# Kernel optimization log

Hardware: AMD Instinct MI355X
Metric: run time of the kernel (lower is better)

Reference implementation:

```python
import jax, jax.numpy as jnp
from jax import lax
import numpy as np

D_MODEL = 1024
D_STATE = 16
D_CONV = 4
EXPAND = 2
D_INNER = EXPAND * D_MODEL          # 2048
DT_RANK = (D_MODEL + 15) // 16      # 64
B_SZ, SEQ = 2, 2048


def setup_inputs() -> dict:
    key = jax.random.key(0)
    ks = jax.random.split(key, 10)
    s = 0.02
    x = jax.random.normal(ks[0], (B_SZ, SEQ, D_MODEL), jnp.float32)
    ln_w = jnp.ones((D_MODEL,), jnp.float32)
    ln_b = jnp.zeros((D_MODEL,), jnp.float32)
    in_proj_w = jax.random.normal(ks[1], (2 * D_INNER, D_MODEL), jnp.float32) * s
    conv_w = jax.random.normal(ks[2], (D_INNER, 1, D_CONV), jnp.float32) * s
    conv_b = jnp.zeros((D_INNER,), jnp.float32)
    x_proj_w = jax.random.normal(ks[3], (DT_RANK + 2 * D_STATE, D_INNER), jnp.float32) * s
    dt_proj_w = jax.random.normal(ks[4], (D_INNER, DT_RANK), jnp.float32) * s
    dt_proj_b = jax.random.normal(ks[5], (D_INNER,), jnp.float32) * s
    # standard Mamba S4D-real init: A = -[1..d_state] per channel
    A_log = jnp.log(jnp.tile(jnp.arange(1, D_STATE + 1, dtype=jnp.float32), (D_INNER, 1)))
    D_param = jnp.ones((D_INNER,), jnp.float32)
    out_proj_w = jax.random.normal(ks[6], (D_MODEL, D_INNER), jnp.float32) * s
    return dict(x=x, ln_w=ln_w, ln_b=ln_b, in_proj_w=in_proj_w, conv_w=conv_w,
                conv_b=conv_b, x_proj_w=x_proj_w, dt_proj_w=dt_proj_w,
                dt_proj_b=dt_proj_b, A_log=A_log, D_param=D_param,
                out_proj_w=out_proj_w)


def _mamba_layer(x, ln_w, ln_b, in_proj_w, conv_w, conv_b, x_proj_w,
                 dt_proj_w, dt_proj_b, A_log, D_param, out_proj_w):
    # LayerNorm (eps=1e-5)
    mu = x.mean(-1, keepdims=True)
    var = ((x - mu) ** 2).mean(-1, keepdims=True)
    xn = (x - mu) * lax.rsqrt(var + 1e-5) * ln_w + ln_b

    # input projection -> gate + conv branch
    xz = jnp.einsum('bld,ed->ble', xn, in_proj_w)  # [B,L,2*D_INNER]
    x_in, z = jnp.split(xz, 2, axis=-1)

    # causal depthwise conv1d + SiLU
    xc = lax.conv_general_dilated(x_in.transpose(0, 2, 1), conv_w, (1,),
                                  [(D_CONV - 1, 0)],
                                  dimension_numbers=('NCH', 'OIH', 'NCH'),
                                  feature_group_count=D_INNER)
    xc = jax.nn.silu(xc + conv_b[None, :, None]).transpose(0, 2, 1)  # [B,L,D_INNER]

    # SSM parameters
    dbl = jnp.einsum('bld,ed->ble', xc, x_proj_w)  # [B,L,DT_RANK+2N]
    dt, Bm, Cm = jnp.split(dbl, [DT_RANK, DT_RANK + D_STATE], axis=-1)
    delta = jax.nn.softplus(jnp.einsum('blr,dr->bld', dt, dt_proj_w) + dt_proj_b)
    A = -jnp.exp(A_log)  # [D_INNER, D_STATE]

    # selective scan over time
    def step(h, inp):
        d_t, B_t, C_t, u_t = inp  # [B,D_INNER],[B,N],[B,N],[B,D_INNER]
        dA = jnp.exp(d_t[..., None] * A)                         # [B,D_INNER,N]
        h = dA * h + (d_t * u_t)[..., None] * B_t[:, None, :]    # [B,D_INNER,N]
        y = jnp.einsum('bdn,bn->bd', h, C_t)
        return h, y

    h0 = jnp.zeros((x.shape[0], D_INNER, D_STATE), x.dtype)
    _, ys = lax.scan(step, h0, (delta.transpose(1, 0, 2), Bm.transpose(1, 0, 2),
                                Cm.transpose(1, 0, 2), xc.transpose(1, 0, 2)))
    y = ys.transpose(1, 0, 2) + xc * D_param   # [B,L,D_INNER]

    y = y * jax.nn.silu(z)
    out = jnp.einsum('ble,de->bld', y, out_proj_w)
    # dropout p=0 (eval) -> identity; residual
    return x + out


def reference(x, ln_w, ln_b, in_proj_w, conv_w, conv_b, x_proj_w,
              dt_proj_w, dt_proj_b, A_log, D_param, out_proj_w):
    return _mamba_layer(x, ln_w, ln_b, in_proj_w, conv_w, conv_b, x_proj_w,
                        dt_proj_w, dt_proj_b, A_log, D_param, out_proj_w)
```

## Files before the change

kernel.cpp:

```cpp
#include <hip/hip_runtime.h>
#include <hip/hip_bf16.h>
#include <math.h>

#define D_MODEL 1024
#define D_INNER 2048
#define DT_RANK 64
#define D_STATE 16
#define BSZ 2
#define SEQ 2048
#define NROW (BSZ * SEQ)
#define NC 128
#define CL (SEQ / NC)
#define NCH (BSZ * D_INNER)
#define KSPLIT 16
#define KCH (D_INNER / KSPLIT)
#define DSPLIT 4

typedef short bf16x8 __attribute__((ext_vector_type(8)));
typedef float f32x4 __attribute__((ext_vector_type(4)));

__device__ inline ushort f2bf(float f) {
    uint32_t u = __float_as_uint(f);
    return (ushort)((u + 0x7FFFu + ((u >> 16) & 1u)) >> 16);
}
__device__ inline float bf2f(ushort u) {
    return __uint_as_float(((uint32_t)u) << 16);
}

__device__ inline void gld_lds16(const void* g, void* l) {
    __builtin_amdgcn_global_load_lds(
        (__attribute__((address_space(1))) void*)g,
        (__attribute__((address_space(3))) void*)l, 16, 0, 0);
}

#define CVT_N1 (2 * D_INNER * D_MODEL / 4)
#define CVT_N2 (D_MODEL * D_INNER / 4)
#define CVT_N3 (D_INNER * DT_RANK / 4)
__global__ __launch_bounds__(256) void cvt_all(const float* __restrict__ a,
                                               const float* __restrict__ b,
                                               const float* __restrict__ c,
                                               ushort* __restrict__ oa,
                                               ushort* __restrict__ ob,
                                               ushort* __restrict__ oc) {
    int i = blockIdx.x * 256 + threadIdx.x;
    const float* src; ushort* dst; int j;
    if (i < CVT_N1)               { src = a; dst = oa; j = i; }
    else if (i < CVT_N1 + CVT_N2) { src = b; dst = ob; j = i - CVT_N1; }
    else                          { src = c; dst = oc; j = i - CVT_N1 - CVT_N2; }
    float4 v = ((const float4*)src)[j];
    ushort4 o;
    o.x = f2bf(v.x); o.y = f2bf(v.y); o.z = f2bf(v.z); o.w = f2bf(v.w);
    ((ushort4*)dst)[j] = o;
}

__global__ __launch_bounds__(256) void ln_kernel(const float* __restrict__ x,
                                                 const float* __restrict__ w,
                                                 const float* __restrict__ b,
                                                 ushort* __restrict__ xn) {
    int row = blockIdx.x;
    int tid = threadIdx.x;
    const float4* xr = (const float4*)(x + (size_t)row * D_MODEL);
    float4 v = xr[tid];
    float s  = v.x + v.y + v.z + v.w;
    float ss = v.x * v.x + v.y * v.y + v.z * v.z + v.w * v.w;
#pragma unroll
    for (int o = 32; o > 0; o >>= 1) {
        s  += __shfl_down(s, o);
        ss += __shfl_down(ss, o);
    }
    __shared__ float red[8];
    int wid = tid >> 6, lane = tid & 63;
    if (lane == 0) { red[wid] = s; red[4 + wid] = ss; }
    __syncthreads();
    s  = red[0] + red[1] + red[2] + red[3];
    ss = red[4] + red[5] + red[6] + red[7];
    float mu  = s * (1.0f / D_MODEL);
    float var = ss * (1.0f / D_MODEL) - mu * mu;
    float inv = rsqrtf(var + 1e-5f);
    float4 wv = ((const float4*)w)[tid];
    float4 bv = ((const float4*)b)[tid];
    ushort4 o4;
    o4.x = f2bf((v.x - mu) * inv * wv.x + bv.x);
    o4.y = f2bf((v.y - mu) * inv * wv.y + bv.y);
    o4.z = f2bf((v.z - mu) * inv * wv.z + bv.z);
    o4.w = f2bf((v.w - mu) * inv * wv.w + bv.w);
    ((ushort4*)(xn + (size_t)row * D_MODEL))[tid] = o4;
}

template <int MODE>
__global__ __launch_bounds__(256) void gemm_mfma(
    const ushort* __restrict__ A, int lda,
    const ushort* __restrict__ B, int ldb,
    float* __restrict__ C, ushort* __restrict__ Z0, ushort* __restrict__ Z1,
    int ldc, int splitN, const float* __restrict__ extra, int K, size_t zstride) {
    __shared__ ushort lds[2][2][128 * 32];
    int tid = threadIdx.x;
    int w = tid >> 6, lane = tid & 63;

    int nwg = gridDim.x * gridDim.y;
    int bid = blockIdx.y * gridDim.x + blockIdx.x;
    int cpx = nwg >> 3;
    int swz = (bid & 7) * cpx + (bid >> 3);
    int bx = swz % gridDim.x, by = swz / gridDim.x;
    int bm = by * 128, bn = bx * 128;
    int wr = w >> 1, wc = w & 1;

    int kofs = (MODE == 3) ? blockIdx.z * K : 0;
    int srow = tid >> 2, sseg = (tid & 3) << 3;
    const ushort* Abase = A + (size_t)(bm + srow) * lda + sseg + kofs;
    const ushort* Bbase = B + (size_t)(bn + srow) * ldb + sseg + kofs;
    int l0 = w * 512;

    int frow = lane & 15, fk = (lane >> 4) << 3;
    f32x4 acc[4][4] = {};

#define STAGE(buf, k0)                                                        \
    do {                                                                      \
        gld_lds16(Abase + (k0),                     &lds[buf][0][l0]);        \
        gld_lds16(Abase + (size_t)64 * lda + (k0),  &lds[buf][0][2048 + l0]); \
        gld_lds16(Bbase + (k0),                     &lds[buf][1][l0]);        \
        gld_lds16(Bbase + (size_t)64 * ldb + (k0),  &lds[buf][1][2048 + l0]); \
    } while (0)

    int nk = K >> 5;
    int cur = 0;
    STAGE(0, 0);
    __syncthreads();
    for (int kt = 0; kt < nk; ++kt) {
        if (kt + 1 < nk) STAGE(cur ^ 1, (kt + 1) << 5);
        bf16x8 a[4], b[4];
#pragma unroll
        for (int m = 0; m < 4; ++m)
            a[m] = *(const bf16x8*)&lds[cur][0][(wr * 64 + m * 16 + frow) * 32 + fk];
#pragma unroll
        for (int n = 0; n < 4; ++n)
            b[n] = *(const bf16x8*)&lds[cur][1][(wc * 64 + n * 16 + frow) * 32 + fk];
#pragma unroll
        for (int m = 0; m < 4; ++m)
#pragma unroll
            for (int n = 0; n < 4; ++n)
                acc[m][n] = __builtin_amdgcn_mfma_f32_16x16x32_bf16(a[m], b[n], acc[m][n], 0, 0, 0);
        __syncthreads();
        cur ^= 1;
    }
#undef STAGE

    float* Cz = (MODE == 3) ? (C + (size_t)blockIdx.z * zstride) : C;
    int rbase = bm + wr * 64 + ((lane >> 4) << 2);
    int cbase = bn + wc * 64 + (lane & 15);
#pragma unroll
    for (int m = 0; m < 4; ++m) {
#pragma unroll
        for (int n = 0; n < 4; ++n) {
            int gc = cbase + n * 16;
#pragma unroll
            for (int j = 0; j < 4; ++j) {
                int gr = rbase + m * 16 + j;
                float v = acc[m][n][j];
                if (MODE == 0) {
                    if (gc < splitN) Z0[(size_t)gr * ldc + gc] = f2bf(v);
                    else             Z1[(size_t)gr * ldc + (gc - splitN)] = f2bf(v);
                } else if (MODE == 1) {
                    v += extra[gc];
                    v = (v > 20.f) ? v : log1pf(__expf(v));
                    Z0[(size_t)gr * ldc + gc] = f2bf(v);
                } else if (MODE == 2) {
                    C[(size_t)gr * ldc + gc] = v + extra[(size_t)gr * ldc + gc];
                } else {
                    Cz[(size_t)gr * ldc + gc] = v;
                }
            }
        }
    }
}

__global__ __launch_bounds__(256) void gemm_d_reduce(const float* __restrict__ part,
                                                     const float* __restrict__ x,
                                                     float* __restrict__ out) {
    int i = blockIdx.x * 256 + threadIdx.x;
    float4 s = ((const float4*)x)[i];
#pragma unroll
    for (int z = 0; z < DSPLIT; ++z) {
        float4 p = ((const float4*)(part + (size_t)z * (NROW * D_MODEL)))[i];
        s.x += p.x; s.y += p.y; s.z += p.z; s.w += p.w;
    }
    ((float4*)out)[i] = s;
}

#define BM 64
#define BN 64
#define BK 16
__global__ __launch_bounds__(256) void gemm_b_split(const ushort* __restrict__ A,
                                                    const float* __restrict__ B,
                                                    float* __restrict__ part) {
    __shared__ float As[BK][BM];
    __shared__ float Bs[BK][BN];
    int bm = blockIdx.y * BM, bn = blockIdx.x * BN;
    int kc = blockIdx.z;
    int tid = threadIdx.x;
    int tx = tid & 15, ty = tid >> 4;
    int lrow = tid >> 2, lseg = (tid & 3) << 2;
    float acc[4][4] = {};

    int kbeg = kc * KCH;
    for (int k0 = kbeg; k0 < kbeg + KCH; k0 += BK) {
        ushort4 au = *(const ushort4*)(A + (size_t)(bm + lrow) * D_INNER + k0 + lseg);
        float4 av = make_float4(bf2f(au.x), bf2f(au.y), bf2f(au.z), bf2f(au.w));
        float4 bv = make_float4(0.f, 0.f, 0.f, 0.f);
        int bgr = bn + lrow;
        if (bgr < 96) bv = *(const float4*)(B + (size_t)bgr * D_INNER + k0 + lseg);
        __syncthreads();
        As[lseg + 0][lrow] = av.x; As[lseg + 1][lrow] = av.y;
        As[lseg + 2][lrow] = av.z; As[lseg + 3][lrow] = av.w;
        Bs[lseg + 0][lrow] = bv.x; Bs[lseg + 1][lrow] = bv.y;
        Bs[lseg + 2][lrow] = bv.z; Bs[lseg + 3][lrow] = bv.w;
        __syncthreads();
#pragma unroll
        for (int k = 0; k < BK; ++k) {
            float4 a4 = *(const float4*)&As[k][ty << 2];
            float4 b4 = *(const float4*)&Bs[k][tx << 2];
            float ar[4] = {a4.x, a4.y, a4.z, a4.w};
            float br[4] = {b4.x, b4.y, b4.z, b4.w};
#pragma unroll
            for (int i = 0; i < 4; ++i)
#pragma unroll
                for (int j = 0; j < 4; ++j) acc[i][j] += ar[i] * br[j];
        }
    }

    float* po = part + (size_t)kc * (NROW * 96);
#pragma unroll
    for (int i = 0; i < 4; ++i) {
        int gr = bm + (ty << 2) + i;
#pragma unroll
        for (int j = 0; j < 4; ++j) {
            int gc = bn + (tx << 2) + j;
            if (gc < 96) po[(size_t)gr * 96 + gc] = acc[i][j];
        }
    }
}

__global__ __launch_bounds__(256) void gemm_b_reduce(const float* __restrict__ part,
                                                     ushort* __restrict__ dbl) {
    int i = blockIdx.x * 256 + threadIdx.x;
    float s = 0.f;
#pragma unroll
    for (int kc = 0; kc < KSPLIT; ++kc)
        s += part[(size_t)kc * (NROW * 96) + i];
    dbl[i] = f2bf(s);
}

__global__ __launch_bounds__(256) void conv_silu(const ushort* __restrict__ xin,
                                                 const float* __restrict__ w,
                                                 const float* __restrict__ cb,
                                                 ushort* __restrict__ xc) {
    int idx = blockIdx.x * 256 + threadIdx.x;
    int d4 = idx & 511;
    int m  = idx >> 9;
    int l  = m & (SEQ - 1);
    int d  = d4 << 2;
    float4 w0 = ((const float4*)w)[d + 0];
    float4 w1 = ((const float4*)w)[d + 1];
    float4 w2 = ((const float4*)w)[d + 2];
    float4 w3 = ((const float4*)w)[d + 3];
    float wr0[4] = {w0.x, w0.y, w0.z, w0.w};
    float wr1[4] = {w1.x, w1.y, w1.z, w1.w};
    float wr2[4] = {w2.x, w2.y, w2.z, w2.w};
    float wr3[4] = {w3.x, w3.y, w3.z, w3.w};
    float ax = cb[d], ay = cb[d + 1], az = cb[d + 2], aw = cb[d + 3];
#pragma unroll
    for (int j = 0; j < 4; ++j) {
        if (l - 3 + j >= 0) {
            ushort4 xu = *(const ushort4*)(xin + (size_t)(m - 3 + j) * D_INNER + d);
            ax += wr0[j] * bf2f(xu.x);
            ay += wr1[j] * bf2f(xu.y);
            az += wr2[j] * bf2f(xu.z);
            aw += wr3[j] * bf2f(xu.w);
        }
    }
    ushort4 o;
    o.x = f2bf(ax / (1.f + __expf(-ax)));
    o.y = f2bf(ay / (1.f + __expf(-ay)));
    o.z = f2bf(az / (1.f + __expf(-az)));
    o.w = f2bf(aw / (1.f + __expf(-aw)));
    *(ushort4*)(xc + (size_t)m * D_INNER + d) = o;
}

#define EXP4(e, cj) \
    e.x = __expf(dt * cj.x); e.y = __expf(dt * cj.y); \
    e.z = __expf(dt * cj.z); e.w = __expf(dt * cj.w);
#define HUPD(hj, cj, Bv) { float4 e; EXP4(e, cj) \
    hj.x = e.x * hj.x + du * Bv.x; hj.y = e.y * hj.y + du * Bv.y; \
    hj.z = e.z * hj.z + du * Bv.z; hj.w = e.w * hj.w + du * Bv.w; }

__global__ __launch_bounds__(256) void scan_phase1(const ushort* __restrict__ delta,
                                                   const ushort* __restrict__ xc,
                                                   const ushort* __restrict__ dbl,
                                                   const float* __restrict__ A_log,
                                                   float* __restrict__ S,
                                                   float* __restrict__ sumdt) {
    __shared__ float bs[CL][16];
    int tid = threadIdx.x;
    int g = blockIdx.x * 256 + tid;
    int c = g & (NCH - 1);
    int k = g >> 12;
    int d = c & (D_INNER - 1);
    int b = c >> 11;
    size_t r0 = (size_t)b * SEQ + (size_t)k * CL;

    if (tid < CL * 4) {
        int t = tid >> 2, j = (tid & 3) << 2;
        ushort4 u4 = *(const ushort4*)(dbl + (r0 + t) * 96 + DT_RANK + j);
        bs[t][j + 0] = bf2f(u4.x); bs[t][j + 1] = bf2f(u4.y);
        bs[t][j + 2] = bf2f(u4.z); bs[t][j + 3] = bf2f(u4.w);
    }

    const float4* al = (const float4*)(A_log + d * D_STATE);
    float4 c0 = al[0], c1 = al[1], c2 = al[2], c3 = al[3];
    c0.x = -__expf(c0.x); c0.y = -__expf(c0.y); c0.z = -__expf(c0.z); c0.w = -__expf(c0.w);
    c1.x = -__expf(c1.x); c1.y = -__expf(c1.y); c1.z = -__expf(c1.z); c1.w = -__expf(c1.w);
    c2.x = -__expf(c2.x); c2.y = -__expf(c2.y); c2.z = -__expf(c2.z); c2.w = -__expf(c2.w);
    c3.x = -__expf(c3.x); c3.y = -__expf(c3.y); c3.z = -__expf(c3.z); c3.w = -__expf(c3.w);
    __syncthreads();

    const ushort* pd = delta + r0 * D_INNER + d;
    const ushort* pu = xc    + r0 * D_INNER + d;
    float4 h0 = {}, h1 = {}, h2 = {}, h3 = {};
    float sdt = 0.f;
#pragma unroll 4
    for (int t = 0; t < CL; ++t) {
        float dt = bf2f(*pd), u = bf2f(*pu);
        float4 B0 = *(const float4*)&bs[t][0];
        float4 B1 = *(const float4*)&bs[t][4];
        float4 B2 = *(const float4*)&bs[t][8];
        float4 B3 = *(const float4*)&bs[t][12];
        float du = dt * u;
        sdt += dt;
        HUPD(h0, c0, B0) HUPD(h1, c1, B1) HUPD(h2, c2, B2) HUPD(h3, c3, B3)
        pd += D_INNER; pu += D_INNER;
    }
    float4* So = (float4*)(S + ((size_t)g << 4));
    So[0] = h0; So[1] = h1; So[2] = h2; So[3] = h3;
    sumdt[g] = sdt;
}

__global__ __launch_bounds__(256) void scan_phase2(float* __restrict__ S,
                                                   const float* __restrict__ sumdt,
                                                   const float* __restrict__ A_log) {
    int g = blockIdx.x * 256 + threadIdx.x;
    int n = g & 15;
    int c = g >> 4;
    int d = c & (D_INNER - 1);
    float cn = -__expf(A_log[d * D_STATE + n]);
    float h = 0.f;
#pragma unroll 8
    for (int k = 0; k < NC; ++k) {
        int kc = (k << 12) | c;
        float P = __expf(sumdt[kc] * cn);
        size_t o = ((size_t)kc << 4) + n;
        float s = S[o];
        S[o] = h;
        h = P * h + s;
    }
}

__global__ __launch_bounds__(256) void scan_phase3(const ushort* __restrict__ delta,
                                                   const ushort* __restrict__ xc,
                                                   const ushort* __restrict__ dbl,
                                                   const ushort* __restrict__ zb,
                                                   const float* __restrict__ A_log,
                                                   const float* __restrict__ Dp,
                                                   const float* __restrict__ hin,
                                                   ushort* __restrict__ y) {
    __shared__ float bcs[CL][32];
    int tid = threadIdx.x;
    int g = blockIdx.x * 256 + tid;
    int c = g & (NCH - 1);
    int k = g >> 12;
    int d = c & (D_INNER - 1);
    int b = c >> 11;
    size_t r0 = (size_t)b * SEQ + (size_t)k * CL;

    if (tid < CL * 8) {
        int t = tid >> 3, j = (tid & 7) << 2;
        ushort4 u4 = *(const ushort4*)(dbl + (r0 + t) * 96 + DT_RANK + j);
        bcs[t][j + 0] = bf2f(u4.x); bcs[t][j + 1] = bf2f(u4.y);
        bcs[t][j + 2] = bf2f(u4.z); bcs[t][j + 3] = bf2f(u4.w);
    }

    const float4* al = (const float4*)(A_log + d * D_STATE);
    float4 c0 = al[0], c1 = al[1], c2 = al[2], c3 = al[3];
    c0.x = -__expf(c0.x); c0.y = -__expf(c0.y); c0.z = -__expf(c0.z); c0.w = -__expf(c0.w);
    c1.x = -__expf(c1.x); c1.y = -__expf(c1.y); c1.z = -__expf(c1.z); c1.w = -__expf(c1.w);
    c2.x = -__expf(c2.x); c2.y = -__expf(c2.y); c2.z = -__expf(c2.z); c2.w = -__expf(c2.w);
    c3.x = -__expf(c3.x); c3.y = -__expf(c3.y); c3.z = -__expf(c3.z); c3.w = -__expf(c3.w);
    float Dv = Dp[d];
    const float4* hi = (const float4*)(hin + ((size_t)g << 4));
    float4 h0 = hi[0], h1 = hi[1], h2 = hi[2], h3 = hi[3];
    __syncthreads();

    const ushort* pd = delta + r0 * D_INNER + d;
    const ushort* pu = xc    + r0 * D_INNER + d;
    const ushort* pz = zb    + r0 * D_INNER + d;
    ushort* py = y           + r0 * D_INNER + d;
#pragma unroll 4
    for (int t = 0; t < CL; ++t) {
        float dt = bf2f(*pd), u = bf2f(*pu);
        float4 B0 = *(const float4*)&bcs[t][0];
        float4 B1 = *(const float4*)&bcs[t][4];
        float4 B2 = *(const float4*)&bcs[t][8];
        float4 B3 = *(const float4*)&bcs[t][12];
        float4 C0 = *(const float4*)&bcs[t][16];
        float4 C1 = *(const float4*)&bcs[t][20];
        float4 C2 = *(const float4*)&bcs[t][24];
        float4 C3 = *(const float4*)&bcs[t][28];
        float du = dt * u;
        HUPD(h0, c0, B0) HUPD(h1, c1, B1) HUPD(h2, c2, B2) HUPD(h3, c3, B3)
        float acc = h0.x * C0.x + h0.y * C0.y + h0.z * C0.z + h0.w * C0.w
                  + h1.x * C1.x + h1.y * C1.y + h1.z * C1.z + h1.w * C1.w
                  + h2.x * C2.x + h2.y * C2.y + h2.z * C2.z + h2.w * C2.w
                  + h3.x * C3.x + h3.y * C3.y + h3.z * C3.z + h3.w * C3.w;
        float zv = bf2f(*pz);
        float sz = zv / (1.f + __expf(-zv));
        *py = f2bf((acc + u * Dv) * sz);
        pd += D_INNER; pu += D_INNER; pz += D_INNER; py += D_INNER;
    }
}

extern "C" void kernel_launch(void* const* d_in, const int* in_sizes, int n_in,
                              void* d_out, int out_size, void* d_ws, size_t ws_size,
                              hipStream_t stream) {
    const float* x       = (const float*)d_in[0];
    const float* ln_w    = (const float*)d_in[1];
    const float* ln_b    = (const float*)d_in[2];
    const float* in_proj = (const float*)d_in[3];
    const float* conv_w  = (const float*)d_in[4];
    const float* conv_b  = (const float*)d_in[5];
    const float* x_proj  = (const float*)d_in[6];
    const float* dt_w    = (const float*)d_in[7];
    const float* dt_b    = (const float*)d_in[8];
    const float* A_log   = (const float*)d_in[9];
    const float* Dp      = (const float*)d_in[10];
    const float* out_w   = (const float*)d_in[11];
    float* out = (float*)d_out;

    char* ws = (char*)d_ws;
    const size_t MB = 1024ull * 1024ull;
    ushort* xn_bf    = (ushort*)(ws);
    ushort* w_in_bf  = (ushort*)(ws + 8 * MB);
    float*  Shin     = (float*)(ws);
    float*  part_d   = (float*)(ws);
    ushort* x_in_bf  = (ushort*)(ws + 16 * MB);
    ushort* zbuf_bf  = (ushort*)(ws + 32 * MB);
    ushort* xc_bf    = (ushort*)(ws + 48 * MB);
    ushort* dbl_bf   = (ushort*)(ws + 64 * MB);
    ushort* dt_w_bf  = (ushort*)(ws + 65 * MB);
    ushort* delta_bf = (ushort*)(ws + 66 * MB);
    ushort* y_bf     = (ushort*)(ws + 82 * MB);
    float*  sumdt    = (float*)(ws + 98 * MB);
    float*  part_b   = (float*)(ws + 100 * MB);
    ushort* w_out_bf = (ushort*)(ws + 124 * MB);

    cvt_all<<<(CVT_N1 + CVT_N2 + CVT_N3) / 256, 256, 0, stream>>>(
        in_proj, out_w, dt_w, w_in_bf, w_out_bf, dt_w_bf);

    ln_kernel<<<NROW, 256, 0, stream>>>(x, ln_w, ln_b, xn_bf);

    gemm_mfma<0><<<dim3(4096 / 128, NROW / 128), 256, 0, stream>>>(
        xn_bf, D_MODEL, w_in_bf, D_MODEL, nullptr, x_in_bf, zbuf_bf,
        D_INNER, D_INNER, nullptr, D_MODEL, 0);

    conv_silu<<<(NROW * (D_INNER / 4)) / 256, 256, 0, stream>>>(x_in_bf, conv_w, conv_b, xc_bf);

    gemm_b_split<<<dim3(2, NROW / BM, KSPLIT), 256, 0, stream>>>(xc_bf, x_proj, part_b);
    gemm_b_reduce<<<(NROW * 96) / 256, 256, 0, stream>>>(part_b, dbl_bf);

    gemm_mfma<1><<<dim3(D_INNER / 128, NROW / 128), 256, 0, stream>>>(
        dbl_bf, 96, dt_w_bf, DT_RANK, nullptr, delta_bf, nullptr,
        D_INNER, 0, dt_b, DT_RANK, 0);

    scan_phase1<<<(NCH * NC) / 256, 256, 0, stream>>>(
        delta_bf, xc_bf, dbl_bf, A_log, Shin, sumdt);
    scan_phase2<<<(NCH * D_STATE) / 256, 256, 0, stream>>>(Shin, sumdt, A_log);
    scan_phase3<<<(NCH * NC) / 256, 256, 0, stream>>>(
        delta_bf, xc_bf, dbl_bf, zbuf_bf, A_log, Dp, Shin, y_bf);

    gemm_mfma<3><<<dim3(D_MODEL / 128, NROW / 128, DSPLIT), 256, 0, stream>>>(
        y_bf, D_INNER, w_out_bf, D_INNER, part_d, nullptr, nullptr,
        D_MODEL, 0, nullptr, D_INNER / DSPLIT, (size_t)NROW * D_MODEL);
    gemm_d_reduce<<<(NROW * D_MODEL / 4) / 256, 256, 0, stream>>>(part_d, x, out);
}
```

Measured before the change: 389.5 us.

## Swap MFMA operands for vectorized GEMM epilogue stores and drop tile swizzle

Swaps the A/B operands of the MFMA so each lane's four accumulator values run along the output column dimension rather than rows. The epilogue can then write ushort4/float4 vectors instead of scalar strided stores, and read the bias and residual with vector loads. It also removes the block-index swizzle in favour of plain row-major tile mapping, which may change L2 locality across workgroups.

```diff
diff --git a/kernel.cpp b/kernel.cpp
--- a/kernel.cpp
+++ b/kernel.cpp
@@ -96,13 +96,7 @@
     __shared__ ushort lds[2][2][128 * 32];
     int tid = threadIdx.x;
     int w = tid >> 6, lane = tid & 63;
-
-    int nwg = gridDim.x * gridDim.y;
-    int bid = blockIdx.y * gridDim.x + blockIdx.x;
-    int cpx = nwg >> 3;
-    int swz = (bid & 7) * cpx + (bid >> 3);
-    int bx = swz % gridDim.x, by = swz / gridDim.x;
-    int bm = by * 128, bn = bx * 128;
+    int bm = blockIdx.y * 128, bn = blockIdx.x * 128;
     int wr = w >> 1, wc = w & 1;
 
     int kofs = (MODE == 3) ? blockIdx.z * K : 0;
@@ -139,36 +133,44 @@
         for (int m = 0; m < 4; ++m)
 #pragma unroll
             for (int n = 0; n < 4; ++n)
-                acc[m][n] = __builtin_amdgcn_mfma_f32_16x16x32_bf16(a[m], b[n], acc[m][n], 0, 0, 0);
+                acc[m][n] = __builtin_amdgcn_mfma_f32_16x16x32_bf16(b[n], a[m], acc[m][n], 0, 0, 0);
         __syncthreads();
         cur ^= 1;
     }
 #undef STAGE
 
     float* Cz = (MODE == 3) ? (C + (size_t)blockIdx.z * zstride) : C;
-    int rbase = bm + wr * 64 + ((lane >> 4) << 2);
-    int cbase = bn + wc * 64 + (lane & 15);
+    int rbase = bm + wr * 64 + (lane & 15);
+    int cbase = bn + wc * 64 + ((lane >> 4) << 2);
 #pragma unroll
     for (int m = 0; m < 4; ++m) {
+        int gr = rbase + m * 16;
 #pragma unroll
         for (int n = 0; n < 4; ++n) {
             int gc = cbase + n * 16;
-#pragma unroll
-            for (int j = 0; j < 4; ++j) {
-                int gr = rbase + m * 16 + j;
-                float v = acc[m][n][j];
-                if (MODE == 0) {
-                    if (gc < splitN) Z0[(size_t)gr * ldc + gc] = f2bf(v);
-                    else             Z1[(size_t)gr * ldc + (gc - splitN)] = f2bf(v);
-                } else if (MODE == 1) {
-                    v += extra[gc];
-                    v = (v > 20.f) ? v : log1pf(__expf(v));
-                    Z0[(size_t)gr * ldc + gc] = f2bf(v);
-                } else if (MODE == 2) {
-                    C[(size_t)gr * ldc + gc] = v + extra[(size_t)gr * ldc + gc];
-                } else {
-                    Cz[(size_t)gr * ldc + gc] = v;
-                }
+            f32x4 v = acc[m][n];
+            if (MODE == 0) {
+                ushort4 o;
+                o.x = f2bf(v[0]); o.y = f2bf(v[1]); o.z = f2bf(v[2]); o.w = f2bf(v[3]);
+                if (gc < splitN) *(ushort4*)&Z0[(size_t)gr * ldc + gc] = o;
+                else             *(ushort4*)&Z1[(size_t)gr * ldc + (gc - splitN)] = o;
+            } else if (MODE == 1) {
+                float4 e = *(const float4*)&extra[gc];
+                float r0 = v[0] + e.x, r1 = v[1] + e.y, r2 = v[2] + e.z, r3 = v[3] + e.w;
+                r0 = (r0 > 20.f) ? r0 : log1pf(__expf(r0));
+                r1 = (r1 > 20.f) ? r1 : log1pf(__expf(r1));
+                r2 = (r2 > 20.f) ? r2 : log1pf(__expf(r2));
+                r3 = (r3 > 20.f) ? r3 : log1pf(__expf(r3));
+                ushort4 o;
+                o.x = f2bf(r0); o.y = f2bf(r1); o.z = f2bf(r2); o.w = f2bf(r3);
+                *(ushort4*)&Z0[(size_t)gr * ldc + gc] = o;
+            } else if (MODE == 2) {
+                float4 e = *(const float4*)&extra[(size_t)gr * ldc + gc];
+                float4 o = make_float4(v[0] + e.x, v[1] + e.y, v[2] + e.z, v[3] + e.w);
+                *(float4*)&C[(size_t)gr * ldc + gc] = o;
+            } else {
+                float4 o = make_float4(v[0], v[1], v[2], v[3]);
+                *(float4*)&Cz[(size_t)gr * ldc + gc] = o;
             }
         }
     }
```

After: 473.7 us. 21.6% more time.
